# Kernel tuning notes

Measured on AMD Instinct MI355X. Metric: run time of the kernel, lower is better.

## Reference

```python
import jax, jax.numpy as jnp
import numpy as np

# DenseKAN defaults from tfkan
GRID_SIZE = 5
SPLINE_ORDER = 3
GRID_MIN, GRID_MAX = -1.0, 1.0
KH = KW = 3  # kernel_size


def _grid():
    h = (GRID_MAX - GRID_MIN) / GRID_SIZE
    # grid_size + 2*spline_order + 1 knots, extended beyond grid_range
    return jnp.linspace(GRID_MIN - SPLINE_ORDER * h, GRID_MAX + SPLINE_ORDER * h,
                        GRID_SIZE + 2 * SPLINE_ORDER + 1, dtype=jnp.float32)


def _spline_basis(x, grid, order):
    # x: (N, in_size) -> (N, in_size, grid_size + spline_order) via Cox-de Boor
    x = x[..., None]
    b = ((x >= grid[:-1]) & (x < grid[1:])).astype(x.dtype)
    for k in range(1, order + 1):
        b = ((x - grid[:-(k + 1)]) / (grid[k:-1] - grid[:-(k + 1)]) * b[..., :-1]
             + (grid[k + 1:] - x) / (grid[k + 1:] - grid[1:-k]) * b[..., 1:])
    return b


def _extract_patches(x):
    # VALID, stride 1; TF extract_patches flattens feature dim as [kh, kw, C]
    B, H, W, C = x.shape
    Ho, Wo = H - KH + 1, W - KW + 1
    p = jnp.stack([x[:, di:di + Ho, dj:dj + Wo, :]
                   for di in range(KH) for dj in range(KW)], axis=3)  # (B,Ho,Wo,KH*KW,C)
    return p.reshape(B, Ho, Wo, KH * KW * C)


def setup_inputs() -> dict:
    key = jax.random.key(0)
    k = jax.random.split(key, 5)
    B, H, W, C = 32, 32, 32, 32
    F = 128
    in_size = KH * KW * C
    basis = GRID_SIZE + SPLINE_ORDER
    return {
        "x": jax.random.normal(k[0], (B, H, W, C), jnp.float32),
        "spline_kernel": jax.random.normal(k[1], (in_size, basis, F), jnp.float32) * 0.1,
        "scale_factor": jax.random.normal(k[2], (in_size, F), jnp.float32) * 0.1,
        "kan_bias": jnp.zeros((F,), jnp.float32),
        "conv_bias": jnp.zeros((F,), jnp.float32),
    }


def reference(x, spline_kernel, scale_factor, kan_bias, conv_bias):
    grid = _grid()
    pat = _extract_patches(x)                 # (B, Ho, Wo, in_size)
    B, Ho, Wo, In = pat.shape
    xf = pat.reshape(-1, In)                  # (N, in_size)
    sb = _spline_basis(xf, grid, SPLINE_ORDER)  # (N, in_size, basis)
    # phi(x) = scale * (spline(x) + silu(x)); output = sum_i phi_i + biases
    # fused: never materialize the (N, in_size, units) tensor
    w = spline_kernel * scale_factor[:, None, :]        # (in_size, basis, units)
    out = (jnp.einsum('nik,iko->no', sb, w)
           + jax.nn.silu(xf) @ scale_factor
           + kan_bias)                                   # (N, units)
    out = out.reshape(B, Ho, Wo, -1) + conv_bias
    return out
```

## Files before the change

kernel.cpp:

```cpp
#include <hip/hip_runtime.h>
#include <hip/hip_bf16.h>


#define C_IN   32
#define F_OUT  128
#define BATCH  32
#define HIN    32
#define WIN    32
#define HO_    30
#define WO_    30
#define NPIX   (BATCH*HO_*WO_)
#define NELEM  (BATCH*HIN*WIN*C_IN)
#define NBASIS 9
#define KCHUNKS 81
#define FEAT_BYTES  ((size_t)NELEM*NBASIS*2)
#define WPACK_BYTES ((size_t)KCHUNKS*F_OUT*32*2)

typedef __attribute__((ext_vector_type(8))) short short8;
typedef __attribute__((ext_vector_type(4))) float f32x4;

#define GLOAD_LDS16(g, l) \
  __builtin_amdgcn_global_load_lds((const __attribute__((address_space(1))) void*)(g), \
                                   (__attribute__((address_space(3))) void*)(l), 16, 0, 0)

__global__ __launch_bounds__(256) void kan_featurize(
    const float* __restrict__ x, __hip_bfloat16* __restrict__ feat) {
  int idx = blockIdx.x * 256 + threadIdx.x;
  float v = x[idx];

  float b0[11], b1[10], b2[9], b3[8];
#pragma unroll
  for (int j = 0; j < 11; ++j) {
    float gj  = -2.2f + 0.4f * (float)j;
    float gj1 = -2.2f + 0.4f * (float)(j + 1);
    b0[j] = (v >= gj && v < gj1) ? 1.0f : 0.0f;
  }
#pragma unroll
  for (int j = 0; j < 10; ++j) {
    float gj = -2.2f + 0.4f * (float)j;
    b1[j] = (v - gj) * 2.5f * b0[j] + ((gj + 0.8f) - v) * 2.5f * b0[j + 1];
  }
#pragma unroll
  for (int j = 0; j < 9; ++j) {
    float gj = -2.2f + 0.4f * (float)j;
    b2[j] = (v - gj) * 1.25f * b1[j] + ((gj + 1.2f) - v) * 1.25f * b1[j + 1];
  }
#pragma unroll
  for (int j = 0; j < 8; ++j) {
    float gj = -2.2f + 0.4f * (float)j;
    b3[j] = (v - gj) * (1.0f/1.2f) * b2[j] + ((gj + 1.6f) - v) * (1.0f/1.2f) * b2[j + 1];
  }
  float sil = v / (1.0f + __expf(-v));

  int bhw = idx >> 5, c = idx & 31;
  __hip_bfloat16* o = feat + (size_t)bhw * (NBASIS * 32) + c;
#pragma unroll
  for (int k = 0; k < 8; ++k) o[k * 32] = __float2bfloat16(b3[k]);
  o[8 * 32] = __float2bfloat16(sil);
}

__global__ __launch_bounds__(256) void kan_pack_w(
    const float* __restrict__ sk, const float* __restrict__ sf,
    __hip_bfloat16* __restrict__ wp) {
  int tid = blockIdx.x * 256 + threadIdx.x;
  int csub = tid & 31;
  int col  = (tid >> 5) & 127;
  int kc   = tid >> 12;
  int dd = kc / 9, k = kc - dd * 9;
  int i = dd * 32 + csub;
  float w = sf[i * 128 + col];
  if (k < 8) w *= sk[(i * 8 + k) * 128 + col];
  int part = csub >> 3, within = csub & 7;
  int slot = part ^ ((col >> 1) & 3);
  wp[(size_t)kc * 4096 + col * 32 + slot * 8 + within] = __float2bfloat16(w);
}

__global__ __launch_bounds__(256) void kan_gemm(
    const __hip_bfloat16* __restrict__ featb, const __hip_bfloat16* __restrict__ wpb,
    const float* __restrict__ kbias, const float* __restrict__ cbias,
    float* __restrict__ out) {
  __shared__ char lds[24576];
  const char* feat = (const char*)featb;
  const char* wp   = (const char*)wpb;

  int tid  = threadIdx.x;
  int lane = tid & 63, wid = tid >> 6;
  int wm = wid >> 1, wn = wid & 1;
  int q = lane >> 4, fr = lane & 15;
  int mb = blockIdx.x * 64;

  int arow = tid >> 2, aslot = tid & 3;
  int apix = mb + arow;
  int wo = apix % 30, t30 = apix / 30;
  int ho = t30 % 30,  bb  = t30 / 30;
  const char* asrc = feat + (size_t)((bb * 32 + ho) * 32 + wo) * 576
                          + (size_t)((aslot ^ ((arow >> 1) & 3)) * 16);

  int ar0 = 32 * wm + fr, ar1 = ar0 + 16;
  int aoff0 = ar0 * 64 + ((q ^ ((ar0 >> 1) & 3)) * 16);
  int aoff1 = ar1 * 64 + ((q ^ ((ar1 >> 1) & 3)) * 16);
  int boff[4];
#pragma unroll
  for (int n = 0; n < 4; ++n) {
    int col = 64 * wn + 16 * n + fr;
    boff[n] = col * 64 + ((q ^ ((col >> 1) & 3)) * 16);
  }

  f32x4 acc[2][4];
#pragma unroll
  for (int m = 0; m < 2; ++m)
#pragma unroll
    for (int n = 0; n < 4; ++n) acc[m][n] = (f32x4)(0.0f);

  auto stage = [&](int buf, int kc) {
    int dd = kc / 9, k = kc - dd * 9;
    int di = dd / 3, dj = dd - di * 3;
    int au = (di * 32 + dj) * 576 + k * 64;
    GLOAD_LDS16(asrc + au, lds + buf * 4096 + tid * 16);
    const char* wsrc = wp + (size_t)kc * 8192 + tid * 16;
    GLOAD_LDS16(wsrc,        lds + 8192 + buf * 8192 + tid * 16);
    GLOAD_LDS16(wsrc + 4096, lds + 8192 + buf * 8192 + 4096 + tid * 16);
  };

  stage(0, 0);
  asm volatile("s_waitcnt vmcnt(0)" ::: "memory");
  __syncthreads();

  for (int kc = 0; kc < KCHUNKS; ++kc) {
    int cur = kc & 1;
    if (kc + 1 < KCHUNKS) stage(cur ^ 1, kc + 1);
    const char* A = lds + cur * 4096;
    const char* B = lds + 8192 + cur * 8192;
    short8 a0 = *(const short8*)(A + aoff0);
    short8 a1 = *(const short8*)(A + aoff1);
#pragma unroll
    for (int n = 0; n < 4; ++n) {
      short8 bn = *(const short8*)(B + boff[n]);
      acc[0][n] = __builtin_amdgcn_mfma_f32_16x16x32_bf16(a0, bn, acc[0][n], 0, 0, 0);
      acc[1][n] = __builtin_amdgcn_mfma_f32_16x16x32_bf16(a1, bn, acc[1][n], 0, 0, 0);
    }
    asm volatile("s_waitcnt vmcnt(0)" ::: "memory");
    __syncthreads();
  }

#pragma unroll
  for (int n = 0; n < 4; ++n) {
    int col = 64 * wn + 16 * n + fr;
    float bias = kbias[col] + cbias[col];
#pragma unroll
    for (int m = 0; m < 2; ++m) {
      int row = mb + 32 * wm + 16 * m + q * 4;
      f32x4 v = acc[m][n];
#pragma unroll
      for (int r = 0; r < 4; ++r)
        out[(size_t)(row + r) * 128 + col] = v[r] + bias;
    }
  }
}

extern "C" void kernel_launch(void* const* d_in, const int* in_sizes, int n_in,
                              void* d_out, int out_size, void* d_ws, size_t ws_size,
                              hipStream_t stream) {
  const float* x  = (const float*)d_in[0];
  const float* sk = (const float*)d_in[1];
  const float* sf = (const float*)d_in[2];
  const float* kb = (const float*)d_in[3];
  const float* cb = (const float*)d_in[4];
  float* out = (float*)d_out;

  char* ws = (char*)d_ws;
  __hip_bfloat16* feat = (__hip_bfloat16*)ws;
  __hip_bfloat16* wpk  = (__hip_bfloat16*)(ws + FEAT_BYTES);

  hipLaunchKernelGGL(kan_featurize, dim3(NELEM / 256), dim3(256), 0, stream, x, feat);
  hipLaunchKernelGGL(kan_pack_w, dim3((KCHUNKS * F_OUT * 32) / 256), dim3(256), 0, stream,
                     sk, sf, wpk);
  hipLaunchKernelGGL(kan_gemm, dim3(NPIX / 64), dim3(256), 0, stream,
                     feat, wpk, kb, cb, out);
}
```

Before: 115.3 us.

## Deepen GEMM LDS pipeline to four stages and remap blocks across XCDs

The GEMM's LDS staging grows from a double buffer to a four-slot ring with three chunks in flight. The wait becomes a partial vmcnt(6) with raw s_barrier, so global-to-LDS loads overlap more MFMA work and the per-iteration full drain goes away. Block indices are also remapped so that each XCD handles a contiguous range of pixel tiles, which should improve L2 reuse of overlapping patch rows. The cost is doubled LDS per block (48KB), which may cut occupancy.

Measured after the change: 112.1 us. 1.03x faster.

```diff
diff --git a/kernel.cpp b/kernel.cpp
--- a/kernel.cpp
+++ b/kernel.cpp
@@ -79,7 +79,7 @@
     const __hip_bfloat16* __restrict__ featb, const __hip_bfloat16* __restrict__ wpb,
     const float* __restrict__ kbias, const float* __restrict__ cbias,
     float* __restrict__ out) {
-  __shared__ char lds[24576];
+  __shared__ char lds[49152];
   const char* feat = (const char*)featb;
   const char* wp   = (const char*)wpb;
 
@@ -87,7 +87,11 @@
   int lane = tid & 63, wid = tid >> 6;
   int wm = wid >> 1, wn = wid & 1;
   int q = lane >> 4, fr = lane & 15;
-  int mb = blockIdx.x * 64;
+
+  int orig = blockIdx.x;
+  int xcd = orig & 7, sub = orig >> 3;
+  int swz = (xcd < 2 ? xcd * 57 : 114 + (xcd - 2) * 56) + sub;
+  int mb = swz * 64;
 
   int arow = tid >> 2, aslot = tid & 3;
   int apix = mb + arow;
@@ -112,25 +116,20 @@
 #pragma unroll
     for (int n = 0; n < 4; ++n) acc[m][n] = (f32x4)(0.0f);
 
-  auto stage = [&](int buf, int kc) {
+  auto stage = [&](int kc) {
+    int s = kc & 3;
     int dd = kc / 9, k = kc - dd * 9;
     int di = dd / 3, dj = dd - di * 3;
     int au = (di * 32 + dj) * 576 + k * 64;
-    GLOAD_LDS16(asrc + au, lds + buf * 4096 + tid * 16);
+    GLOAD_LDS16(asrc + au, lds + s * 4096 + tid * 16);
     const char* wsrc = wp + (size_t)kc * 8192 + tid * 16;
-    GLOAD_LDS16(wsrc,        lds + 8192 + buf * 8192 + tid * 16);
-    GLOAD_LDS16(wsrc + 4096, lds + 8192 + buf * 8192 + 4096 + tid * 16);
+    GLOAD_LDS16(wsrc,        lds + 16384 + s * 8192 + tid * 16);
+    GLOAD_LDS16(wsrc + 4096, lds + 16384 + s * 8192 + 4096 + tid * 16);
   };
 
-  stage(0, 0);
-  asm volatile("s_waitcnt vmcnt(0)" ::: "memory");
-  __syncthreads();
-
-  for (int kc = 0; kc < KCHUNKS; ++kc) {
-    int cur = kc & 1;
-    if (kc + 1 < KCHUNKS) stage(cur ^ 1, kc + 1);
-    const char* A = lds + cur * 4096;
-    const char* B = lds + 8192 + cur * 8192;
+  auto compute = [&](int s) {
+    const char* A = lds + s * 4096;
+    const char* B = lds + 16384 + s * 8192;
     short8 a0 = *(const short8*)(A + aoff0);
     short8 a1 = *(const short8*)(A + aoff1);
 #pragma unroll
@@ -139,9 +138,26 @@
       acc[0][n] = __builtin_amdgcn_mfma_f32_16x16x32_bf16(a0, bn, acc[0][n], 0, 0, 0);
       acc[1][n] = __builtin_amdgcn_mfma_f32_16x16x32_bf16(a1, bn, acc[1][n], 0, 0, 0);
     }
-    asm volatile("s_waitcnt vmcnt(0)" ::: "memory");
-    __syncthreads();
+  };
+
+  stage(0); stage(1); stage(2);
+  asm volatile("s_waitcnt vmcnt(6)" ::: "memory");
+  __builtin_amdgcn_s_barrier();
+  __builtin_amdgcn_sched_barrier(0);
+
+  for (int kc = 0; kc < KCHUNKS - 3; ++kc) {
+    stage(kc + 3);
+    compute(kc & 3);
+    asm volatile("s_waitcnt vmcnt(6) lgkmcnt(0)" ::: "memory");
+    __builtin_amdgcn_s_barrier();
+    __builtin_amdgcn_sched_barrier(0);
   }
+  asm volatile("s_waitcnt vmcnt(0)" ::: "memory");
+  __builtin_amdgcn_s_barrier();
+  __builtin_amdgcn_sched_barrier(0);
+  compute((KCHUNKS - 3) & 3);
+  compute((KCHUNKS - 2) & 3);
+  compute((KCHUNKS - 1) & 3);
 
 #pragma unroll
   for (int n = 0; n < 4; ++n) {
```
